# Optimization experiments

Hardware: AMD Instinct MI355X
Metric: run time of the kernel (lower is better)

Reference implementation:

```python
import jax, jax.numpy as jnp
import numpy as np

RADIUS = 0.07          # gno_config.gno_radius
SCALES = (1.0, 2.0)    # gno_config.scales


def _kernel_mlp(pair, kW1, kb1, kW2, kb2, kW3, kb3):
    # ChannelMLP inside IntegralTransform: gelu between layers, none after last
    h = jax.nn.gelu(pair @ kW1 + kb1)
    h = jax.nn.gelu(h @ kW2 + kb2)
    return h @ kW3 + kb3


def setup_inputs() -> dict:
    key = jax.random.key(0)
    ks = jax.random.split(key, 8)
    B, N, NL, CD, IN_C, C, H = 2, 2048, 512, 2, 16, 32, 32

    def glorot(k, shape):
        return jax.random.normal(k, shape) / jnp.sqrt(jnp.float32(shape[0]))

    return {
        "x_coord": jax.random.uniform(ks[0], (B, N, CD), dtype=jnp.float32),
        "pndata": jax.random.normal(ks[1], (B, N, IN_C), dtype=jnp.float32),
        "latent_tokens_coord": jax.random.uniform(ks[2], (NL, CD), dtype=jnp.float32),
        # lifting ChannelMLP (n_layers=1 -> single 1x1 conv == linear)
        "W_lift": glorot(ks[3], (IN_C, C)),
        "b_lift": jnp.zeros((C,), jnp.float32),
        # kernel MLP: [2*coord_dim=4] -> 32 -> 32 -> out_channels=32
        "kW1": glorot(ks[4], (2 * CD, H)),
        "kb1": jnp.zeros((H,), jnp.float32),
        "kW2": glorot(ks[5], (H, H)),
        "kb2": jnp.zeros((H,), jnp.float32),
        "kW3": glorot(ks[6], (H, C)),
        "kb3": jnp.zeros((C,), jnp.float32),
    }


def reference(x_coord, pndata, latent_tokens_coord,
              W_lift, b_lift, kW1, kb1, kW2, kb2, kW3, kb3):
    # lifting: [B,N,in_c] -> [B,N,C]
    f = pndata @ W_lift + b_lift

    B, N, CD = x_coord.shape
    NL = latent_tokens_coord.shape[0]

    y = x_coord[:, None, :, :]                      # [B,1,N,CD] source coords
    xq = latent_tokens_coord[None, :, None, :]      # [1,NL,1,CD] query coords
    # kernel input = cat(y_j, x_i) per (query i, source j) pair -> [B,NL,N,2*CD]
    pair = jnp.concatenate([jnp.broadcast_to(y, (B, NL, N, CD)),
                            jnp.broadcast_to(xq, (B, NL, N, CD))], axis=-1)
    kvals = _kernel_mlp(pair, kW1, kb1, kW2, kb2, kW3, kb3)  # [B,NL,N,C]

    d2 = jnp.sum((y - xq) ** 2, axis=-1)            # [B,NL,N] squared distances

    out = jnp.zeros((B, NL, kvals.shape[-1]), f.dtype)
    for s in SCALES:  # fixed small set of scales (2)
        # radius neighbor search expressed as dense mask (faithful to ball query)
        mask = (d2 <= (RADIUS * s) ** 2).astype(f.dtype)      # [B,NL,N]
        cnt = jnp.maximum(jnp.sum(mask, axis=-1), 1.0)        # [B,NL]
        # 'linear' transform: mean_j k(x_i,y_j) * f(y_j) over neighbors
        agg = jnp.einsum('bijc,bjc,bij->bic', kvals, f, mask)
        out = out + agg / cnt[..., None]
    return out  # [B,NL,C]
```

## Files before the change

### kernel.cpp

```cpp
#include <hip/hip_runtime.h>

static constexpr int B_ = 2, N_ = 2048, NL_ = 512, IN_C_ = 16, C_ = 32, H_ = 32;
static constexpr float R1SQ = (float)(0.07 * 0.07);
static constexpr float R2SQ = (float)(0.14 * 0.14);

typedef __attribute__((ext_vector_type(8))) short bf16x8;
typedef __attribute__((ext_vector_type(4))) float f32x4;

__device__ __forceinline__ float gelu_tanh(float x) {
    float z2 = 2.0f * 0.7978845608028654f * x * fmaf(0.044715f * x, x, 1.0f);
    float e = __expf(z2);
    float t = __builtin_amdgcn_rcpf(e + 1.0f);
    return x - x * t;
}

__device__ __forceinline__ short f2bf(float x) {
    unsigned u = __float_as_uint(x);
    u += 0x7fffu + ((u >> 16) & 1u);
    return (short)(u >> 16);
}

__global__ __launch_bounds__(256)
void lift_kernel(const float* __restrict__ pnd,
                 const float* __restrict__ Wl, const float* __restrict__ bl,
                 float* __restrict__ f)
{
    __shared__ float sW[IN_C_ * C_];
    __shared__ float sb[C_];
    int tid = threadIdx.x;
    for (int idx = tid; idx < IN_C_ * C_; idx += 256) sW[idx] = Wl[idx];
    if (tid < C_) sb[tid] = bl[tid];
    __syncthreads();
    int c = tid & 31;
    int row = blockIdx.x * 8 + (tid >> 5);
    if (row >= B_ * N_) return;
    const float* p = pnd + (size_t)row * IN_C_;
    float s = sb[c];
#pragma unroll
    for (int m = 0; m < IN_C_; ++m) s = fmaf(p[m], sW[m * C_ + c], s);
    f[(size_t)row * C_ + c] = s;
}

__global__ __launch_bounds__(256)
void magno_mfma(const float* __restrict__ x_coord,
                const float* __restrict__ lat,
                const float* __restrict__ kW1, const float* __restrict__ kb1,
                const float* __restrict__ kW2, const float* __restrict__ kb2,
                const float* __restrict__ kW3, const float* __restrict__ kb3,
                const float* __restrict__ f,
                float* __restrict__ out)
{
    __shared__ float sW23[2][H_ * H_];
    __shared__ float sR0[H_], sR1[H_], sA1[H_];
    __shared__ unsigned jlist[4][512];
    __shared__ __align__(16) short strans[4][64 * 40];
    __shared__ float sred[4][C_];
    __shared__ int scnt[4][2];

    const int tid  = threadIdx.x;
    const int lane = tid & 63;
    const int wid  = tid >> 6;
    const int qd   = lane >> 4;
    const int li   = lane & 15;
    const int bi = blockIdx.x;
    const int b = bi >> 9, i = bi & (NL_ - 1);
    const float xq0 = lat[2 * i], xq1 = lat[2 * i + 1];

    for (int idx = tid; idx < H_ * H_; idx += 256) {
        sW23[0][idx] = kW2[idx];
        sW23[1][idx] = kW3[idx];
    }
    if (tid < H_) {
        sR0[tid] = kW1[tid];
        sR1[tid] = kW1[H_ + tid];
        sA1[tid] = fmaf(xq0, kW1[2 * H_ + tid], fmaf(xq1, kW1[3 * H_ + tid], kb1[tid]));
    }
    const float b2A = kb2[li], b2B = kb2[li + 16];
    const float b3A = kb3[li], b3B = kb3[li + 16];

    const float2* __restrict__ xc = (const float2*)(x_coord + (size_t)b * N_ * 2);
    const unsigned long long ltmask = (1ull << lane) - 1ull;
    float2 ys[8];
#pragma unroll
    for (int t = 0; t < 8; ++t) ys[t] = xc[512 * wid + 64 * t + lane];
    int cnt = 0, c1w = 0;
#pragma unroll
    for (int t = 0; t < 8; ++t) {
        float dy0 = ys[t].x - xq0, dy1 = ys[t].y - xq1;
        float d2 = dy0 * dy0 + dy1 * dy1;
        bool in2 = d2 <= R2SQ;
        bool in1 = d2 <= R1SQ;
        unsigned long long m2 = __ballot(in2);
        unsigned long long m1 = __ballot(in1);
        if (in2) {
            int pos = cnt + __popcll(m2 & ltmask);
            jlist[wid][pos] = (unsigned)(512 * wid + 64 * t + lane) | (in1 ? 0x80000000u : 0u);
        }
        cnt += __popcll(m2);
        c1w += __popcll(m1);
    }
    if (lane == 0) { scnt[wid][0] = cnt; scnt[wid][1] = c1w; }
    __syncthreads();

    const int n   = scnt[0][0] + scnt[1][0] + scnt[2][0] + scnt[3][0];
    const int c1  = scnt[0][1] + scnt[1][1] + scnt[2][1] + scnt[3][1];
    int nmax = scnt[0][0];
    nmax = scnt[1][0] > nmax ? scnt[1][0] : nmax;
    nmax = scnt[2][0] > nmax ? scnt[2][0] : nmax;
    nmax = scnt[3][0] > nmax ? scnt[3][0] : nmax;
    const float inv2 = 1.0f / (float)(n  > 0 ? n  : 1);
    const float inv1 = 1.0f / (float)(c1 > 0 ? c1 : 1);
    const int nIter = (nmax + 63) >> 6;

    bf16x8 w2f[2], w3f[2];
#pragma unroll
    for (int nt = 0; nt < 2; ++nt) {
        int n0 = li + 16 * nt;
#pragma unroll
        for (int jj = 0; jj < 8; ++jj) {
            int k = qd * 8 + jj;
            w2f[nt][jj] = f2bf(sW23[0][k * H_ + n0]);
            w3f[nt][jj] = f2bf(sW23[1][k * H_ + n0]);
        }
    }

    float r0v[8], r1v[8], a1v[8];
#pragma unroll
    for (int jj = 0; jj < 8; ++jj) {
        int k = qd * 8 + jj;
        r0v[jj] = sR0[k]; r1v[jj] = sR1[k]; a1v[jj] = sA1[k];
    }

    short* tb = &strans[wid][0];
    const unsigned* __restrict__ jl = &jlist[wid][0];
    const float* __restrict__ fbase = f + (size_t)b * N_ * C_;

    float accA = 0.0f, accB = 0.0f;

    for (int it = 0; it < nIter; ++it) {
        const int base = it * 64;
        const bool active = (base < cnt);

        bf16x8 h2f[4];
        float fAv[4][4], fBv[4][4];
        if (active) {
#pragma unroll
            for (int mt = 0; mt < 4; ++mt)
#pragma unroll
                for (int r = 0; r < 4; ++r) {
                    int el = base + 16 * mt + 4 * qd + r;
                    unsigned pk = jl[el & 511];
                    int j = (int)(pk & (unsigned)(N_ - 1));
                    const float* fr = fbase + (size_t)j * C_;
                    fAv[mt][r] = fr[li];
                    fBv[mt][r] = fr[li + 16];
                }

            bf16x8 hfrag[4];
#pragma unroll
            for (int mt = 0; mt < 4; ++mt) {
                int e = base + 16 * mt + li;
                unsigned pk = jl[e & 511];
                int j = (int)(pk & (unsigned)(N_ - 1));
                float2 y = xc[j];
#pragma unroll
                for (int jj = 0; jj < 8; ++jj)
                    hfrag[mt][jj] = f2bf(gelu_tanh(fmaf(y.x, r0v[jj], fmaf(y.y, r1v[jj], a1v[jj]))));
            }

            f32x4 acc2[4][2];
#pragma unroll
            for (int mt = 0; mt < 4; ++mt)
#pragma unroll
                for (int nt = 0; nt < 2; ++nt) {
                    f32x4 z = {0.f, 0.f, 0.f, 0.f};
                    acc2[mt][nt] = __builtin_amdgcn_mfma_f32_16x16x32_bf16(hfrag[mt], w2f[nt], z, 0, 0, 0);
                }

#pragma unroll
            for (int mt = 0; mt < 4; ++mt)
#pragma unroll
                for (int nt = 0; nt < 2; ++nt) {
                    float bb = nt ? b2B : b2A;
                    int hid = li + 16 * nt;
#pragma unroll
                    for (int r = 0; r < 4; ++r) {
                        int entry = 16 * mt + 4 * qd + r;
                        tb[entry * 40 + hid] = f2bf(gelu_tanh(acc2[mt][nt][r] + bb));
                    }
                }
        }
        __syncthreads();
        if (active) {
#pragma unroll
            for (int mt = 0; mt < 4; ++mt)
                h2f[mt] = *(const bf16x8*)&tb[(li + 16 * mt) * 40 + qd * 8];
        }
        __syncthreads();
        if (active) {
            f32x4 acc3[4][2];
#pragma unroll
            for (int mt = 0; mt < 4; ++mt)
#pragma unroll
                for (int nt = 0; nt < 2; ++nt) {
                    f32x4 z = {0.f, 0.f, 0.f, 0.f};
                    acc3[mt][nt] = __builtin_amdgcn_mfma_f32_16x16x32_bf16(h2f[mt], w3f[nt], z, 0, 0, 0);
                }
#pragma unroll
            for (int mt = 0; mt < 4; ++mt)
#pragma unroll
                for (int r = 0; r < 4; ++r) {
                    int el = base + 16 * mt + 4 * qd + r;
                    unsigned pk = jl[el & 511];
                    float w = (el < cnt) ? (inv2 + ((pk & 0x80000000u) ? inv1 : 0.0f)) : 0.0f;
                    accA = fmaf(w * fAv[mt][r], acc3[mt][0][r] + b3A, accA);
                    accB = fmaf(w * fBv[mt][r], acc3[mt][1][r] + b3B, accB);
                }
        }
    }

    accA += __shfl_xor(accA, 16, 64);
    accA += __shfl_xor(accA, 32, 64);
    accB += __shfl_xor(accB, 16, 64);
    accB += __shfl_xor(accB, 32, 64);
    if (lane < 16) {
        sred[wid][li] = accA;
        sred[wid][li + 16] = accB;
    }
    __syncthreads();
    if (tid < C_)
        out[(size_t)bi * C_ + tid] = (sred[0][tid] + sred[1][tid]) + (sred[2][tid] + sred[3][tid]);
}

extern "C" void kernel_launch(void* const* d_in, const int* in_sizes, int n_in,
                              void* d_out, int out_size, void* d_ws, size_t ws_size,
                              hipStream_t stream) {
    const float* x_coord = (const float*)d_in[0];
    const float* pndata  = (const float*)d_in[1];
    const float* lat     = (const float*)d_in[2];
    const float* W_lift  = (const float*)d_in[3];
    const float* b_lift  = (const float*)d_in[4];
    const float* kW1     = (const float*)d_in[5];
    const float* kb1     = (const float*)d_in[6];
    const float* kW2     = (const float*)d_in[7];
    const float* kb2     = (const float*)d_in[8];
    const float* kW3     = (const float*)d_in[9];
    const float* kb3     = (const float*)d_in[10];
    float* out = (float*)d_out;

    float* f = (float*)d_ws;
    lift_kernel<<<(B_ * N_ + 7) / 8, 256, 0, stream>>>(pndata, W_lift, b_lift, f);
    magno_mfma<<<B_ * NL_, 256, 0, stream>>>(
        x_coord, lat, kW1, kb1, kW2, kb2, kW3, kb3, f, out);
}
```

Baseline: 92.23 us.

## Fuse lifting into the neighbor kernel via MFMA and drop block barriers

Removes the separate lift kernel and recomputes each neighbor's lifted features inside the main kernel with a bf16 MFMA on gathered pndata rows. This saves one launch and the round trip of the feature buffer through global memory. Each wave now loops only over its own neighbor count, and the two __syncthreads around the per-wave transpose buffer are gone because that buffer is private to the wave. Weights are pre-converted to bf16 in shared memory and launch bounds request higher occupancy. The cost is redundant lift work per query and some extra precision loss from bf16 lifting.

```diff
diff --git a/kernel.cpp b/kernel.cpp
--- a/kernel.cpp
+++ b/kernel.cpp
@@ -20,37 +20,20 @@
     return (short)(u >> 16);
 }
 
-__global__ __launch_bounds__(256)
-void lift_kernel(const float* __restrict__ pnd,
-                 const float* __restrict__ Wl, const float* __restrict__ bl,
-                 float* __restrict__ f)
+__global__ __launch_bounds__(256, 4)
+void magno_fused(const float* __restrict__ x_coord,
+                 const float* __restrict__ lat,
+                 const float* __restrict__ kW1, const float* __restrict__ kb1,
+                 const float* __restrict__ kW2, const float* __restrict__ kb2,
+                 const float* __restrict__ kW3, const float* __restrict__ kb3,
+                 const float* __restrict__ pnd,
+                 const float* __restrict__ Wl,
+                 const float* __restrict__ bl,
+                 float* __restrict__ out)
 {
-    __shared__ float sW[IN_C_ * C_];
-    __shared__ float sb[C_];
-    int tid = threadIdx.x;
-    for (int idx = tid; idx < IN_C_ * C_; idx += 256) sW[idx] = Wl[idx];
-    if (tid < C_) sb[tid] = bl[tid];
-    __syncthreads();
-    int c = tid & 31;
-    int row = blockIdx.x * 8 + (tid >> 5);
-    if (row >= B_ * N_) return;
-    const float* p = pnd + (size_t)row * IN_C_;
-    float s = sb[c];
-#pragma unroll
-    for (int m = 0; m < IN_C_; ++m) s = fmaf(p[m], sW[m * C_ + c], s);
-    f[(size_t)row * C_ + c] = s;
-}
-
-__global__ __launch_bounds__(256)
-void magno_mfma(const float* __restrict__ x_coord,
-                const float* __restrict__ lat,
-                const float* __restrict__ kW1, const float* __restrict__ kb1,
-                const float* __restrict__ kW2, const float* __restrict__ kb2,
-                const float* __restrict__ kW3, const float* __restrict__ kb3,
-                const float* __restrict__ f,
-                float* __restrict__ out)
-{
-    __shared__ float sW23[2][H_ * H_];
+    __shared__ short sW2b[H_ * H_];
+    __shared__ short sW3b[H_ * C_];
+    __shared__ short sWlb[IN_C_ * C_];
     __shared__ float sR0[H_], sR1[H_], sA1[H_];
     __shared__ unsigned jlist[4][512];
     __shared__ __align__(16) short strans[4][64 * 40];
@@ -66,17 +49,20 @@
     const int b = bi >> 9, i = bi & (NL_ - 1);
     const float xq0 = lat[2 * i], xq1 = lat[2 * i + 1];
 
+    const float b2A = kb2[li], b2B = kb2[li + 16];
+    const float b3A = kb3[li], b3B = kb3[li + 16];
+    const float blA = bl[li],  blB = bl[li + 16];
+
     for (int idx = tid; idx < H_ * H_; idx += 256) {
-        sW23[0][idx] = kW2[idx];
-        sW23[1][idx] = kW3[idx];
-    }
+        sW2b[idx] = f2bf(kW2[idx]);
+        sW3b[idx] = f2bf(kW3[idx]);
+    }
+    for (int idx = tid; idx < IN_C_ * C_; idx += 256) sWlb[idx] = f2bf(Wl[idx]);
     if (tid < H_) {
         sR0[tid] = kW1[tid];
         sR1[tid] = kW1[H_ + tid];
         sA1[tid] = fmaf(xq0, kW1[2 * H_ + tid], fmaf(xq1, kW1[3 * H_ + tid], kb1[tid]));
     }
-    const float b2A = kb2[li], b2B = kb2[li + 16];
-    const float b3A = kb3[li], b3B = kb3[li + 16];
 
     const float2* __restrict__ xc = (const float2*)(x_coord + (size_t)b * N_ * 2);
     const unsigned long long ltmask = (1ull << lane) - 1ull;
@@ -102,15 +88,10 @@
     if (lane == 0) { scnt[wid][0] = cnt; scnt[wid][1] = c1w; }
     __syncthreads();
 
-    const int n   = scnt[0][0] + scnt[1][0] + scnt[2][0] + scnt[3][0];
-    const int c1  = scnt[0][1] + scnt[1][1] + scnt[2][1] + scnt[3][1];
-    int nmax = scnt[0][0];
-    nmax = scnt[1][0] > nmax ? scnt[1][0] : nmax;
-    nmax = scnt[2][0] > nmax ? scnt[2][0] : nmax;
-    nmax = scnt[3][0] > nmax ? scnt[3][0] : nmax;
+    const int n  = scnt[0][0] + scnt[1][0] + scnt[2][0] + scnt[3][0];
+    const int c1 = scnt[0][1] + scnt[1][1] + scnt[2][1] + scnt[3][1];
     const float inv2 = 1.0f / (float)(n  > 0 ? n  : 1);
     const float inv1 = 1.0f / (float)(c1 > 0 ? c1 : 1);
-    const int nIter = (nmax + 63) >> 6;
 
     bf16x8 w2f[2], w3f[2];
 #pragma unroll
@@ -119,104 +100,115 @@
 #pragma unroll
         for (int jj = 0; jj < 8; ++jj) {
             int k = qd * 8 + jj;
-            w2f[nt][jj] = f2bf(sW23[0][k * H_ + n0]);
-            w3f[nt][jj] = f2bf(sW23[1][k * H_ + n0]);
-        }
-    }
-
-    float r0v[8], r1v[8], a1v[8];
-#pragma unroll
-    for (int jj = 0; jj < 8; ++jj) {
-        int k = qd * 8 + jj;
-        r0v[jj] = sR0[k]; r1v[jj] = sR1[k]; a1v[jj] = sA1[k];
+            w2f[nt][jj] = sW2b[k * H_ + n0];
+            w3f[nt][jj] = sW3b[k * C_ + n0];
+        }
     }
 
     short* tb = &strans[wid][0];
     const unsigned* __restrict__ jl = &jlist[wid][0];
-    const float* __restrict__ fbase = f + (size_t)b * N_ * C_;
+    const float* __restrict__ pbase = pnd + (size_t)b * N_ * IN_C_;
 
     float accA = 0.0f, accB = 0.0f;
-
-    for (int it = 0; it < nIter; ++it) {
-        const int base = it * 64;
-        const bool active = (base < cnt);
-
-        bf16x8 h2f[4];
-        float fAv[4][4], fBv[4][4];
-        if (active) {
-#pragma unroll
-            for (int mt = 0; mt < 4; ++mt)
+    const bool pq = (qd < 2);
+
+    for (int base = 0; base < cnt; base += 64) {
+        int jm[4];
+#pragma unroll
+        for (int mt = 0; mt < 4; ++mt) {
+            int e = base + 16 * mt + li;
+            jm[mt] = (int)(jl[e & 511] & (unsigned)(N_ - 1));
+        }
+
+        float4 pv[4][2];
+        if (pq) {
+#pragma unroll
+            for (int mt = 0; mt < 4; ++mt) {
+                const float4* p4 = (const float4*)(pbase + (size_t)jm[mt] * IN_C_ + qd * 8);
+                pv[mt][0] = p4[0];
+                pv[mt][1] = p4[1];
+            }
+        }
+        float2 yv[4];
+#pragma unroll
+        for (int mt = 0; mt < 4; ++mt) yv[mt] = xc[jm[mt]];
+
+        bf16x8 wlf[2];
+#pragma unroll
+        for (int nt = 0; nt < 2; ++nt) {
+            int n0 = li + 16 * nt;
+#pragma unroll
+            for (int jj = 0; jj < 8; ++jj) {
+                int k = qd * 8 + jj;
+                wlf[nt][jj] = pq ? sWlb[k * C_ + n0] : (short)0;
+            }
+        }
+
+        f32x4 accF[4][2];
+#pragma unroll
+        for (int mt = 0; mt < 4; ++mt) {
+            bf16x8 paf;
+            if (pq) {
+                paf[0] = f2bf(pv[mt][0].x); paf[1] = f2bf(pv[mt][0].y);
+                paf[2] = f2bf(pv[mt][0].z); paf[3] = f2bf(pv[mt][0].w);
+                paf[4] = f2bf(pv[mt][1].x); paf[5] = f2bf(pv[mt][1].y);
+                paf[6] = f2bf(pv[mt][1].z); paf[7] = f2bf(pv[mt][1].w);
+            } else {
+#pragma unroll
+                for (int jj = 0; jj < 8; ++jj) paf[jj] = (short)0;
+            }
+            f32x4 z = {0.f, 0.f, 0.f, 0.f};
+            accF[mt][0] = __builtin_amdgcn_mfma_f32_16x16x32_bf16(paf, wlf[0], z, 0, 0, 0);
+            accF[mt][1] = __builtin_amdgcn_mfma_f32_16x16x32_bf16(paf, wlf[1], z, 0, 0, 0);
+        }
+
+        f32x4 acc2[4][2];
+#pragma unroll
+        for (int mt = 0; mt < 4; ++mt) {
+            bf16x8 hfrag;
+#pragma unroll
+            for (int jj = 0; jj < 8; ++jj) {
+                int k = qd * 8 + jj;
+                float h = gelu_tanh(fmaf(yv[mt].x, sR0[k], fmaf(yv[mt].y, sR1[k], sA1[k])));
+                hfrag[jj] = f2bf(h);
+            }
+            f32x4 z = {0.f, 0.f, 0.f, 0.f};
+            acc2[mt][0] = __builtin_amdgcn_mfma_f32_16x16x32_bf16(hfrag, w2f[0], z, 0, 0, 0);
+            acc2[mt][1] = __builtin_amdgcn_mfma_f32_16x16x32_bf16(hfrag, w2f[1], z, 0, 0, 0);
+        }
+
+#pragma unroll
+        for (int mt = 0; mt < 4; ++mt)
+#pragma unroll
+            for (int nt = 0; nt < 2; ++nt) {
+                float bb = nt ? b2B : b2A;
+                int hid = li + 16 * nt;
 #pragma unroll
                 for (int r = 0; r < 4; ++r) {
-                    int el = base + 16 * mt + 4 * qd + r;
-                    unsigned pk = jl[el & 511];
-                    int j = (int)(pk & (unsigned)(N_ - 1));
-                    const float* fr = fbase + (size_t)j * C_;
-                    fAv[mt][r] = fr[li];
-                    fBv[mt][r] = fr[li + 16];
+                    int entry = 16 * mt + 4 * qd + r;
+                    tb[entry * 40 + hid] = f2bf(gelu_tanh(acc2[mt][nt][r] + bb));
                 }
-
-            bf16x8 hfrag[4];
-#pragma unroll
-            for (int mt = 0; mt < 4; ++mt) {
-                int e = base + 16 * mt + li;
-                unsigned pk = jl[e & 511];
-                int j = (int)(pk & (unsigned)(N_ - 1));
-                float2 y = xc[j];
-#pragma unroll
-                for (int jj = 0; jj < 8; ++jj)
-                    hfrag[mt][jj] = f2bf(gelu_tanh(fmaf(y.x, r0v[jj], fmaf(y.y, r1v[jj], a1v[jj]))));
-            }
-
-            f32x4 acc2[4][2];
-#pragma unroll
-            for (int mt = 0; mt < 4; ++mt)
-#pragma unroll
-                for (int nt = 0; nt < 2; ++nt) {
-                    f32x4 z = {0.f, 0.f, 0.f, 0.f};
-                    acc2[mt][nt] = __builtin_amdgcn_mfma_f32_16x16x32_bf16(hfrag[mt], w2f[nt], z, 0, 0, 0);
-                }
-
-#pragma unroll
-            for (int mt = 0; mt < 4; ++mt)
-#pragma unroll
-                for (int nt = 0; nt < 2; ++nt) {
-                    float bb = nt ? b2B : b2A;
-                    int hid = li + 16 * nt;
-#pragma unroll
-                    for (int r = 0; r < 4; ++r) {
-                        int entry = 16 * mt + 4 * qd + r;
-                        tb[entry * 40 + hid] = f2bf(gelu_tanh(acc2[mt][nt][r] + bb));
-                    }
-                }
-        }
-        __syncthreads();
-        if (active) {
-#pragma unroll
-            for (int mt = 0; mt < 4; ++mt)
-                h2f[mt] = *(const bf16x8*)&tb[(li + 16 * mt) * 40 + qd * 8];
-        }
-        __syncthreads();
-        if (active) {
-            f32x4 acc3[4][2];
-#pragma unroll
-            for (int mt = 0; mt < 4; ++mt)
-#pragma unroll
-                for (int nt = 0; nt < 2; ++nt) {
-                    f32x4 z = {0.f, 0.f, 0.f, 0.f};
-                    acc3[mt][nt] = __builtin_amdgcn_mfma_f32_16x16x32_bf16(h2f[mt], w3f[nt], z, 0, 0, 0);
-                }
-#pragma unroll
-            for (int mt = 0; mt < 4; ++mt)
-#pragma unroll
-                for (int r = 0; r < 4; ++r) {
-                    int el = base + 16 * mt + 4 * qd + r;
-                    unsigned pk = jl[el & 511];
-                    float w = (el < cnt) ? (inv2 + ((pk & 0x80000000u) ? inv1 : 0.0f)) : 0.0f;
-                    accA = fmaf(w * fAv[mt][r], acc3[mt][0][r] + b3A, accA);
-                    accB = fmaf(w * fBv[mt][r], acc3[mt][1][r] + b3B, accB);
-                }
-        }
+            }
+
+        f32x4 acc3[4][2];
+#pragma unroll
+        for (int mt = 0; mt < 4; ++mt) {
+            bf16x8 h2 = *(const bf16x8*)&tb[(li + 16 * mt) * 40 + qd * 8];
+            f32x4 z = {0.f, 0.f, 0.f, 0.f};
+            acc3[mt][0] = __builtin_amdgcn_mfma_f32_16x16x32_bf16(h2, w3f[0], z, 0, 0, 0);
+            acc3[mt][1] = __builtin_amdgcn_mfma_f32_16x16x32_bf16(h2, w3f[1], z, 0, 0, 0);
+        }
+
+#pragma unroll
+        for (int mt = 0; mt < 4; ++mt)
+#pragma unroll
+            for (int r = 0; r < 4; ++r) {
+                int el = base + 16 * mt + 4 * qd + r;
+                unsigned pk = jl[el & 511];
+                float w = (el < cnt) ? (inv2 + ((pk & 0x80000000u) ? inv1 : 0.0f)) : 0.0f;
+                accA = fmaf(w * (accF[mt][0][r] + blA), acc3[mt][0][r] + b3A, accA);
+                accB = fmaf(w * (accF[mt][1][r] + blB), acc3[mt][1][r] + b3B, accB);
+            }
     }
 
     accA += __shfl_xor(accA, 16, 64);
@@ -248,8 +240,7 @@
     const float* kb3     = (const float*)d_in[10];
     float* out = (float*)d_out;
 
-    float* f = (float*)d_ws;
-    lift_kernel<<<(B_ * N_ + 7) / 8, 256, 0, stream>>>(pndata, W_lift, b_lift, f);
-    magno_mfma<<<B_ * NL_, 256, 0, stream>>>(
-        x_coord, lat, kW1, kb1, kW2, kb2, kW3, kb3, f, out);
-}
+    magno_fused<<<B_ * NL_, 256, 0, stream>>>(
+        x_coord, lat, kW1, kb1, kW2, kb2, kW3, kb3,
+        pndata, W_lift, b_lift, out);
+}
```

Result: slower. 104.1 us (+12.9%).
